# Performance work log

Hardware: AMD Instinct MI355X
Metric: run time of the kernel (lower is better)

Reference implementation:

```python
import jax, jax.numpy as jnp
import numpy as np

N_ITEMS = 30000
D = 128            # embedding_dim
F = D // 2 + 1     # freq_dim = 65
RAW_IMG = 1024
RAW_TXT = 768


def setup_inputs() -> dict:
    key = jax.random.key(0)
    ks = jax.random.split(key, 13)
    return {
        "image_embeds": jax.random.normal(ks[0], (N_ITEMS, D), jnp.float32),
        "text_embeds": jax.random.normal(ks[1], (N_ITEMS, D), jnp.float32),
        "image_table": jax.random.normal(ks[2], (N_ITEMS, RAW_IMG), jnp.float32),
        "text_table": jax.random.normal(ks[3], (N_ITEMS, RAW_TXT), jnp.float32),
        "W_img": jax.random.normal(ks[4], (RAW_IMG, D), jnp.float32) * 0.02,
        "b_img": jax.random.normal(ks[5], (D,), jnp.float32) * 0.02,
        "W_txt": jax.random.normal(ks[6], (RAW_TXT, D), jnp.float32) * 0.02,
        "b_txt": jax.random.normal(ks[7], (D,), jnp.float32) * 0.02,
        "avrf_img": jax.random.normal(ks[8], (F,), jnp.float32),
        "avrf_txt": jax.random.normal(ks[9], (F,), jnp.float32),
        "avg_R": jax.random.normal(ks[10], (F,), jnp.float32),
        "psi": jax.random.normal(ks[11], (F,), jnp.float32) * 0.1,
        "lambda_weights": jnp.array([0.6, 0.4], jnp.float32),
    }


def reference(image_embeds, text_embeds, image_table, text_table,
              W_img, b_img, W_txt, b_txt,
              avrf_img, avrf_txt, avg_R, psi, lambda_weights):
    # project full embedding tables: [N, raw] @ [raw, D] -> [N, D]
    proj_image = image_table @ W_img + b_img
    proj_txt = text_table @ W_txt + b_txt
    # per-row rFFT -> [N, F] complex
    img_fft = jnp.fft.rfft(proj_image, axis=1, norm="ortho")
    txt_fft = jnp.fft.rfft(proj_txt, axis=1, norm="ortho")
    # phase alignment rotation
    phi = avg_R * 0.5 + psi                      # [F]
    rot = jnp.exp(-1j * phi.astype(jnp.complex64))
    APC_img = img_fft * rot[None, :]
    APC_txt = txt_fft * jnp.conj(rot)[None, :]
    # AVRF (variance-ratio) masking -- torch forward uses the raw logit params
    img_vr = APC_img * avrf_img[None, :]
    txt_vr = APC_txt * avrf_txt[None, :]
    # IMCF: magnitude-squared coherence masking
    cross = APC_img * jnp.conj(APC_txt)
    msc = jnp.abs(cross) ** 2 / (jnp.abs(APC_img) ** 2 * jnp.abs(APC_txt) ** 2 + 1e-8)
    img_imcf = APC_img * msc
    txt_imcf = APC_txt * msc
    # softmax-weighted late fusion of the two filtered spectra
    lam = jax.nn.softmax(lambda_weights)
    img_late = lam[0] * img_vr + lam[1] * img_imcf
    txt_late = lam[0] * txt_vr + lam[1] * txt_imcf
    image_conv = jnp.fft.irfft(img_late, n=image_embeds.shape[1], axis=1, norm="ortho")
    text_conv = jnp.fft.irfft(txt_late, n=text_embeds.shape[1], axis=1, norm="ortho")
    return image_conv, text_conv
```

## Files before the change

### kernel.cpp

```cpp
#include <hip/hip_runtime.h>
#include <math.h>

typedef __bf16 bf16x8 __attribute__((ext_vector_type(8)));
typedef float f32x4 __attribute__((ext_vector_type(4)));
typedef unsigned short u16;
typedef unsigned int u32;

#define S128 0.08838834764831845f
#define TWOPI_128 0.04908738521234052f
#define MROWS 30016

__device__ __align__(16) u16 g_wft[56 * 12288];
__device__ __align__(16) u16 g_gt[6 * 8192];
__device__ __align__(16) float g_fp[96 * 8];
__device__ __align__(16) u32 g_S[(size_t)2 * 6 * 4 * MROWS * 8];

__device__ __forceinline__ void split2(float v, u16& h, u16& l) {
  unsigned u = __float_as_uint(v);
  h = (u16)(u >> 16);
  float hf = __uint_as_float(u & 0xFFFF0000u);
  float lo = v - hf;
  unsigned ul = __float_as_uint(lo);
  l = (u16)((ul + 0x7FFFu + ((ul >> 16) & 1u)) >> 16);
}

__device__ __forceinline__ void gll16(const void* gsrc, void* ldst) {
  __builtin_amdgcn_global_load_lds(
      (const __attribute__((address_space(1))) unsigned int*)gsrc,
      (__attribute__((address_space(3))) unsigned int*)ldst, 16, 0, 0);
}

__global__ void k_setup_wft(const float* __restrict__ Wimg,
                            const float* __restrict__ Wtxt, int Kimg, int Ktxt) {
  int gid = blockIdx.x * 256 + threadIdx.x;
  int imgn = Kimg * 96;
  if (gid >= imgn + Ktxt * 96) return;
  const float* Wrow;
  u16* base;
  int kloc, fq;
  if (gid < imgn) {
    kloc = gid / 96; fq = gid % 96;
    Wrow = Wimg + (size_t)kloc * 128;
    base = g_wft + (size_t)(kloc >> 5) * 12288;
  } else {
    int l = gid - imgn;
    kloc = l / 96; fq = l % 96;
    Wrow = Wtxt + (size_t)kloc * 128;
    base = g_wft + (size_t)(32 + (kloc >> 5)) * 12288;
  }
  float re = 0.f, im = 0.f;
  if (fq <= 64) {
    float sts, stc;
    sincosf(TWOPI_128 * (float)fq, &sts, &stc);
    for (int d0 = 0; d0 < 128; d0 += 16) {
      int m = (fq * d0) & 127;
      float sa, ca;
      sincosf(TWOPI_128 * (float)m, &sa, &ca);
      float cr = ca, ci = -sa;
      float wv[16];
      *(float4*)&wv[0]  = *(const float4*)&Wrow[d0];
      *(float4*)&wv[4]  = *(const float4*)&Wrow[d0 + 4];
      *(float4*)&wv[8]  = *(const float4*)&Wrow[d0 + 8];
      *(float4*)&wv[12] = *(const float4*)&Wrow[d0 + 12];
#pragma unroll
      for (int jj = 0; jj < 16; ++jj) {
        re = fmaf(wv[jj], cr, re);
        im = fmaf(wv[jj], ci, im);
        float nc = cr * stc + ci * sts;
        ci = ci * stc - cr * sts;
        cr = nc;
      }
    }
    re *= S128; im *= S128;
  }
  int gran = (kloc & 31) >> 3, j = kloc & 7;
  int cre = (fq >> 4) * 32 + (fq & 15);
  u16 h, l;
  split2(re, h, l);
  base[gran * 1536 + cre * 8 + j] = h;
  base[6144 + gran * 1536 + cre * 8 + j] = l;
  split2(im, h, l);
  base[gran * 1536 + (cre + 16) * 8 + j] = h;
  base[6144 + gran * 1536 + (cre + 16) * 8 + j] = l;
}

__global__ void k_setup_gt(void) {
  int gid = blockIdx.x * 256 + threadIdx.x;
  if (gid >= 192 * 128) return;
  int pk = gid >> 7, n = gid & 127;
  int ks = pk >> 5, w = pk & 31, gran = (w >> 3) & 3, j = w & 7;
  int part = w >> 4, fl = ks * 16 + (w & 15);
  float val = 0.f;
  if (fl <= 64) {
    float ck = (fl == 0 || fl == 64) ? 1.f : 2.f;
    int m = (fl * n) & 127;
    float sa, ca;
    sincosf(TWOPI_128 * (float)m, &sa, &ca);
    val = (part == 0 ? ca : -sa) * ck * S128;
  }
  u16 h, l;
  split2(val, h, l);
  g_gt[ks * 8192 + gran * 1024 + n * 8 + j] = h;
  g_gt[ks * 8192 + 4096 + gran * 1024 + n * 8 + j] = l;
}

__global__ void k_setup_fp(const float* __restrict__ b_img, const float* __restrict__ b_txt,
                           const float* __restrict__ avrf_img, const float* __restrict__ avrf_txt,
                           const float* __restrict__ avg_R, const float* __restrict__ psi) {
  int gid = blockIdx.x * 256 + threadIdx.x;
  if (gid >= 96 * 4) return;
  int k = gid >> 2, q = gid & 3;
  float* fp = g_fp + k * 8;
  if (k > 64) {
    if (q == 0) { fp[0] = 1.f; fp[1] = 0.f; fp[2] = 0.f; fp[3] = 0.f; }
    fp[4 + q] = 0.f;
    return;
  }
  if (q == 0) {
    float phi = avg_R[k] * 0.5f + psi[k];
    float s, c;
    sincosf(phi, &s, &c);
    fp[0] = c; fp[1] = s; fp[2] = avrf_img[k]; fp[3] = avrf_txt[k];
  }
  const float* b = (q < 2) ? b_img : b_txt;
  int part = q & 1;
  float acc = 0.f;
  for (int d = 0; d < 128; ++d) {
    int m = (k * d) & 127;
    float sa, ca;
    sincosf(TWOPI_128 * (float)m, &sa, &ca);
    acc = fmaf(b[d], part ? -sa : ca, acc);
  }
  fp[4 + q] = acc * S128;
}

__global__ __launch_bounds__(256) void k1_gemm(
    const float* __restrict__ Aimg, const float* __restrict__ Atxt,
    int M, int Kimg, int Ktxt, int bpm) {
  __shared__ __align__(16) u16 Asm[2 * 4096];
  __shared__ __align__(16) u16 Bsm[2 * 6144];

  const int bid = blockIdx.x;
  const int mod = bid >= bpm;
  const int bblk = mod ? bid - bpm : bid;
  const float* A = mod ? Atxt : Aimg;
  const int K = mod ? Ktxt : Kimg;
  const u16* wft = g_wft + (mod ? (size_t)32 * 12288 : 0);
  const int row0 = bblk * 64;

  const int tid = threadIdx.x;
  const int lane = tid & 63, wv = tid >> 6;
  const int la = lane & 15, hh = lane >> 4;
  const int wr = wv >> 1, wc = wv & 1;

  const int rseg = tid >> 2, kseg = (tid & 3) * 8;
  int grow = row0 + rseg;
  if (grow > M - 1) grow = M - 1;
  const float* Abase = A + (size_t)grow * K + kseg;

  f32x4 acc[2][6];
#pragma unroll
  for (int rt = 0; rt < 2; ++rt)
#pragma unroll
    for (int ct = 0; ct < 6; ++ct) acc[rt][ct] = (f32x4){0.f, 0.f, 0.f, 0.f};

  const int nst = K / 32;
  float4 av0 = *(const float4*)(Abase);
  float4 av1 = *(const float4*)(Abase + 4);

  for (int s = 0; s < nst; ++s) {
    __syncthreads();
    {
      u16 h8[8], l8[8];
      const float va[8] = {av0.x, av0.y, av0.z, av0.w, av1.x, av1.y, av1.z, av1.w};
#pragma unroll
      for (int j = 0; j < 8; ++j) split2(va[j], h8[j], l8[j]);
      const int ab = (kseg >> 3) * 512 + rseg * 8;
      *(bf16x8*)&Asm[ab] = *(bf16x8*)h8;
      *(bf16x8*)&Asm[4096 + ab] = *(bf16x8*)l8;
    }
    {
      const u16* src = wft + (size_t)s * 12288;
#pragma unroll
      for (int i = 0; i < 6; ++i)
        gll16(src + i * 2048 + tid * 8, (char*)Bsm + i * 4096 + tid * 16);
    }
    __syncthreads();
    if (s + 1 < nst) {
      av0 = *(const float4*)(Abase + (s + 1) * 32);
      av1 = *(const float4*)(Abase + (s + 1) * 32 + 4);
    }
    bf16x8 fah[2], fal[2];
#pragma unroll
    for (int rt = 0; rt < 2; ++rt) {
      const int ar = wr * 32 + rt * 16 + la;
      fah[rt] = *(const bf16x8*)&Asm[hh * 512 + ar * 8];
      fal[rt] = *(const bf16x8*)&Asm[4096 + hh * 512 + ar * 8];
    }
#pragma unroll
    for (int ct = 0; ct < 6; ++ct) {
      const int col = wc * 96 + ct * 16 + la;
      const u16* bb = &Bsm[hh * 1536 + col * 8];
      const bf16x8 fbh = *(const bf16x8*)bb;
      const bf16x8 fbl = *(const bf16x8*)(bb + 6144);
#pragma unroll
      for (int rt = 0; rt < 2; ++rt) {
        acc[rt][ct] = __builtin_amdgcn_mfma_f32_16x16x32_bf16(fah[rt], fbh, acc[rt][ct], 0, 0, 0);
        acc[rt][ct] = __builtin_amdgcn_mfma_f32_16x16x32_bf16(fah[rt], fbl, acc[rt][ct], 0, 0, 0);
        acc[rt][ct] = __builtin_amdgcn_mfma_f32_16x16x32_bf16(fal[rt], fbh, acc[rt][ct], 0, 0, 0);
      }
    }
  }

#pragma unroll
  for (int ct = 0; ct < 6; ++ct) {
    const int cg = wc * 6 + ct;
    const int fq = (cg >> 1) * 16 + la;
    const float bv = g_fp[fq * 8 + 4 + mod * 2 + (cg & 1)];
    const int ks = cg >> 1;
    const int khh = (cg & 1) * 2 + (la >> 3);
    const int j8 = la & 7;
    const size_t sbase = ((size_t)((mod * 6 + ks) * 4 + khh)) * MROWS;
#pragma unroll
    for (int rt = 0; rt < 2; ++rt) {
      const int rb = row0 + wr * 32 + rt * 16 + hh * 4;
#pragma unroll
      for (int j = 0; j < 4; ++j) {
        u16 h, l;
        split2(acc[rt][ct][j] + bv, h, l);
        g_S[(sbase + rb + j) * 8 + j8] = ((u32)h << 16) | l;
      }
    }
  }
}

__global__ __launch_bounds__(256) void k2_idft(
    const float* __restrict__ lamw, float* __restrict__ out, int M) {
  __shared__ __align__(16) u16 Gs[8192];
  __shared__ __align__(16) float fps[96 * 8];

  const int tid = threadIdx.x;
  const int lane = tid & 63, wv = tid >> 6;
  const int la = lane & 15, hh = lane >> 4;
  const int part = hh >> 1;
  const int row = blockIdx.x * 64 + wv * 16 + la;

  if (tid < 192) gll16((const char*)g_fp + tid * 16, (char*)fps + tid * 16);

  const float l0 = lamw[0], l1 = lamw[1];
  const float mx = fmaxf(l0, l1);
  const float e0 = expf(l0 - mx), e1 = expf(l1 - mx);
  const float lam0 = e0 / (e0 + e1), lam1 = e1 / (e0 + e1);

  f32x4 ai[8], at[8];
#pragma unroll
  for (int ct = 0; ct < 8; ++ct) {
    ai[ct] = (f32x4){0.f, 0.f, 0.f, 0.f};
    at[ct] = (f32x4){0.f, 0.f, 0.f, 0.f};
  }

  for (int ks = 0; ks < 6; ++ks) {
    const u32* si = &g_S[((size_t)((0 + ks) * 4 + hh) * MROWS + row) * 8];
    const u32* st = &g_S[((size_t)((24 + ks * 4) + hh) * MROWS + row) * 8];
    uint4 vi0 = *(const uint4*)si, vi1 = *(const uint4*)(si + 4);
    uint4 vt0 = *(const uint4*)st, vt1 = *(const uint4*)(st + 4);

    __syncthreads();
#pragma unroll
    for (int i = 0; i < 4; ++i)
      gll16((const char*)(g_gt + ks * 8192) + i * 4096 + tid * 16,
            (char*)Gs + i * 4096 + tid * 16);
    __syncthreads();

    u32 vs_i[8], vs_t[8];
    *(uint4*)&vs_i[0] = vi0; *(uint4*)&vs_i[4] = vi1;
    *(uint4*)&vs_t[0] = vt0; *(uint4*)&vs_t[4] = vt1;

    const int fq0 = ks * 16 + (hh & 1) * 8;
    u16 yih[8], yil[8], yth[8], ytl[8];
#pragma unroll
    for (int j = 0; j < 8; ++j) {
      const f32x4 fpv = *(const f32x4*)&fps[(fq0 + j) * 8];
      const float o_i = __uint_as_float(vs_i[j] & 0xFFFF0000u) + __uint_as_float(vs_i[j] << 16);
      const float o_t = __uint_as_float(vs_t[j] & 0xFFFF0000u) + __uint_as_float(vs_t[j] << 16);
      const float p_i = __shfl_xor(o_i, 32);
      const float p_t = __shfl_xor(o_t, 32);
      const float Sre_i = part ? p_i : o_i;
      const float Sim_i = part ? o_i : p_i;
      const float Sre_t = part ? p_t : o_t;
      const float Sim_t = part ? o_t : p_t;
      const float rc = fpv[0], rs = fpv[1];
      const float Air = Sre_i * rc + Sim_i * rs, Aii = Sim_i * rc - Sre_i * rs;
      const float Atr = Sre_t * rc - Sim_t * rs, Ati = Sim_t * rc + Sre_t * rs;
      const float cre = Air * Atr + Aii * Ati, cim = Aii * Atr - Air * Ati;
      const float pa = Air * Air + Aii * Aii, pb = Atr * Atr + Ati * Ati;
      const float msc = (cre * cre + cim * cim) / (pa * pb + 1e-8f);
      const float mi = lam0 * fpv[2] + lam1 * msc;
      const float mt = lam0 * fpv[3] + lam1 * msc;
      const float yi = (part ? Aii : Air) * mi;
      const float yt = (part ? Ati : Atr) * mt;
      split2(yi, yih[j], yil[j]);
      split2(yt, yth[j], ytl[j]);
    }
    const bf16x8 fih = *(bf16x8*)yih, fil = *(bf16x8*)yil;
    const bf16x8 fth = *(bf16x8*)yth, ftl = *(bf16x8*)ytl;
#pragma unroll
    for (int ct = 0; ct < 8; ++ct) {
      const u16* gb = &Gs[hh * 1024 + (ct * 16 + la) * 8];
      const bf16x8 gh = *(const bf16x8*)gb;
      const bf16x8 gl = *(const bf16x8*)(gb + 4096);
      ai[ct] = __builtin_amdgcn_mfma_f32_16x16x32_bf16(fih, gh, ai[ct], 0, 0, 0);
      ai[ct] = __builtin_amdgcn_mfma_f32_16x16x32_bf16(fih, gl, ai[ct], 0, 0, 0);
      ai[ct] = __builtin_amdgcn_mfma_f32_16x16x32_bf16(fil, gh, ai[ct], 0, 0, 0);
      at[ct] = __builtin_amdgcn_mfma_f32_16x16x32_bf16(fth, gh, at[ct], 0, 0, 0);
      at[ct] = __builtin_amdgcn_mfma_f32_16x16x32_bf16(fth, gl, at[ct], 0, 0, 0);
      at[ct] = __builtin_amdgcn_mfma_f32_16x16x32_bf16(ftl, gh, at[ct], 0, 0, 0);
    }
  }

  float* oimg = out;
  float* otxt = out + (size_t)M * 128;
#pragma unroll
  for (int q = 0; q < 4; ++q) {
    const int orow = blockIdx.x * 64 + wv * 16 + hh * 4 + q;
    if (orow < M) {
#pragma unroll
      for (int ct = 0; ct < 8; ++ct) {
        oimg[(size_t)orow * 128 + ct * 16 + la] = ai[ct][q];
        otxt[(size_t)orow * 128 + ct * 16 + la] = at[ct][q];
      }
    }
  }
}

extern "C" void kernel_launch(void* const* d_in, const int* in_sizes, int n_in,
                              void* d_out, int out_size, void* d_ws, size_t ws_size,
                              hipStream_t stream) {
  const float* image_table = (const float*)d_in[2];
  const float* text_table  = (const float*)d_in[3];
  const float* W_img = (const float*)d_in[4];
  const float* b_img = (const float*)d_in[5];
  const float* W_txt = (const float*)d_in[6];
  const float* b_txt = (const float*)d_in[7];
  const float* avrf_img = (const float*)d_in[8];
  const float* avrf_txt = (const float*)d_in[9];
  const float* avg_R = (const float*)d_in[10];
  const float* psi = (const float*)d_in[11];
  const float* lamw = (const float*)d_in[12];

  const int M = in_sizes[0] / 128;
  const int K_img = in_sizes[4] / 128;
  const int K_txt = in_sizes[6] / 128;

  const int wft_threads = (K_img + K_txt) * 96;
  k_setup_wft<<<(wft_threads + 255) / 256, 256, 0, stream>>>(W_img, W_txt, K_img, K_txt);
  k_setup_gt<<<(192 * 128 + 255) / 256, 256, 0, stream>>>();
  k_setup_fp<<<2, 256, 0, stream>>>(b_img, b_txt, avrf_img, avrf_txt, avg_R, psi);

  const int bpm = (M + 63) / 64;
  k1_gemm<<<2 * bpm, 256, 0, stream>>>(image_table, text_table, M, K_img, K_txt, bpm);
  k2_idft<<<bpm, 256, 0, stream>>>(lamw, (float*)d_out, M);
}
```

Baseline: 149.5 us.

## Double-buffer B tiles in GEMM and XOR-swizzle LDS layouts against bank conflicts

The GEMM stage now keeps two B (weight-Fourier) tile buffers in LDS and prefetches the next k-step's tile with async global-to-LDS loads while the current step computes, instead of loading and waiting inside each step. The A tile buffer is halved to a single hi/lo pair. The LDS layouts for A, B and the inverse-DFT matrix G get an XOR swizzle on the granule index, applied consistently in the setup kernels that pre-lay-out the weights, to cut LDS bank conflicts on the bf16x8 fragment reads. This costs more LDS per block, which may lower occupancy.

New measurement: 159.7 us. 6.8% more time.

```diff
diff --git a/kernel.cpp b/kernel.cpp
--- a/kernel.cpp
+++ b/kernel.cpp
@@ -77,11 +77,11 @@
   int cre = (fq >> 4) * 32 + (fq & 15);
   u16 h, l;
   split2(re, h, l);
-  base[gran * 1536 + cre * 8 + j] = h;
-  base[6144 + gran * 1536 + cre * 8 + j] = l;
+  base[(gran * 1536 + cre * 8 + j) ^ (gran << 4)] = h;
+  base[6144 + ((gran * 1536 + cre * 8 + j) ^ (gran << 4))] = l;
   split2(im, h, l);
-  base[gran * 1536 + (cre + 16) * 8 + j] = h;
-  base[6144 + gran * 1536 + (cre + 16) * 8 + j] = l;
+  base[(gran * 1536 + (cre + 16) * 8 + j) ^ (gran << 4)] = h;
+  base[6144 + ((gran * 1536 + (cre + 16) * 8 + j) ^ (gran << 4))] = l;
 }
 
 __global__ void k_setup_gt(void) {
@@ -100,8 +100,8 @@
   }
   u16 h, l;
   split2(val, h, l);
-  g_gt[ks * 8192 + gran * 1024 + n * 8 + j] = h;
-  g_gt[ks * 8192 + 4096 + gran * 1024 + n * 8 + j] = l;
+  g_gt[ks * 8192 + ((gran * 1024 + n * 8 + j) ^ (gran << 4))] = h;
+  g_gt[ks * 8192 + 4096 + ((gran * 1024 + n * 8 + j) ^ (gran << 4))] = l;
 }
 
 __global__ void k_setup_fp(const float* __restrict__ b_img, const float* __restrict__ b_txt,
@@ -137,8 +137,8 @@
 __global__ __launch_bounds__(256) void k1_gemm(
     const float* __restrict__ Aimg, const float* __restrict__ Atxt,
     int M, int Kimg, int Ktxt, int bpm) {
-  __shared__ __align__(16) u16 Asm[2 * 4096];
-  __shared__ __align__(16) u16 Bsm[2 * 6144];
+  __shared__ __align__(16) u16 Asm[4096];
+  __shared__ __align__(16) u16 Bsm[2 * 12288];
 
   const int bid = blockIdx.x;
   const int mod = bid >= bpm;
@@ -153,10 +153,11 @@
   const int la = lane & 15, hh = lane >> 4;
   const int wr = wv >> 1, wc = wv & 1;
 
-  const int rseg = tid >> 2, kseg = (tid & 3) * 8;
+  const int rseg = tid >> 2, g4 = tid & 3;
+  const int awoff = (g4 * 512 + rseg * 8) ^ (g4 << 4);
   int grow = row0 + rseg;
   if (grow > M - 1) grow = M - 1;
-  const float* Abase = A + (size_t)grow * K + kseg;
+  const float* Abase = A + (size_t)grow * K + g4 * 8;
 
   f32x4 acc[2][6];
 #pragma unroll
@@ -165,42 +166,50 @@
     for (int ct = 0; ct < 6; ++ct) acc[rt][ct] = (f32x4){0.f, 0.f, 0.f, 0.f};
 
   const int nst = K / 32;
+
+  auto stageB = [&](int s, int buf) {
+    const u16* src = wft + (size_t)s * 12288;
+    char* dst = (char*)Bsm + buf * 24576;
+#pragma unroll
+    for (int i = 0; i < 6; ++i)
+      gll16(src + i * 2048 + tid * 8, dst + i * 4096 + tid * 16);
+  };
+
+  stageB(0, 0);
   float4 av0 = *(const float4*)(Abase);
   float4 av1 = *(const float4*)(Abase + 4);
 
   for (int s = 0; s < nst; ++s) {
+    const int cur = s & 1;
     __syncthreads();
     {
       u16 h8[8], l8[8];
       const float va[8] = {av0.x, av0.y, av0.z, av0.w, av1.x, av1.y, av1.z, av1.w};
 #pragma unroll
       for (int j = 0; j < 8; ++j) split2(va[j], h8[j], l8[j]);
-      const int ab = (kseg >> 3) * 512 + rseg * 8;
-      *(bf16x8*)&Asm[ab] = *(bf16x8*)h8;
-      *(bf16x8*)&Asm[4096 + ab] = *(bf16x8*)l8;
-    }
-    {
-      const u16* src = wft + (size_t)s * 12288;
-#pragma unroll
-      for (int i = 0; i < 6; ++i)
-        gll16(src + i * 2048 + tid * 8, (char*)Bsm + i * 4096 + tid * 16);
+      *(bf16x8*)&Asm[awoff] = *(bf16x8*)h8;
+      *(bf16x8*)&Asm[2048 + awoff] = *(bf16x8*)l8;
     }
     __syncthreads();
+
     if (s + 1 < nst) {
+      stageB(s + 1, cur ^ 1);
       av0 = *(const float4*)(Abase + (s + 1) * 32);
       av1 = *(const float4*)(Abase + (s + 1) * 32 + 4);
     }
+
     bf16x8 fah[2], fal[2];
 #pragma unroll
     for (int rt = 0; rt < 2; ++rt) {
       const int ar = wr * 32 + rt * 16 + la;
-      fah[rt] = *(const bf16x8*)&Asm[hh * 512 + ar * 8];
-      fal[rt] = *(const bf16x8*)&Asm[4096 + hh * 512 + ar * 8];
+      const int off = (hh * 512 + ar * 8) ^ (hh << 4);
+      fah[rt] = *(const bf16x8*)&Asm[off];
+      fal[rt] = *(const bf16x8*)&Asm[2048 + off];
     }
 #pragma unroll
     for (int ct = 0; ct < 6; ++ct) {
       const int col = wc * 96 + ct * 16 + la;
-      const u16* bb = &Bsm[hh * 1536 + col * 8];
+      const u16* bb = &Bsm[cur * 12288 + ((hh * 1536 + col * 8) ^ (hh << 4))];
       const bf16x8 fbh = *(const bf16x8*)bb;
       const bf16x8 fbl = *(const bf16x8*)(bb + 6144);
 #pragma unroll
@@ -306,9 +315,9 @@
     const bf16x8 fth = *(bf16x8*)yth, ftl = *(bf16x8*)ytl;
 #pragma unroll
     for (int ct = 0; ct < 8; ++ct) {
-      const u16* gb = &Gs[hh * 1024 + (ct * 16 + la) * 8];
-      const bf16x8 gh = *(const bf16x8*)gb;
-      const bf16x8 gl = *(const bf16x8*)(gb + 4096);
+      const int goff = (hh * 1024 + (ct * 16 + la) * 8) ^ (hh << 4);
+      const bf16x8 gh = *(const bf16x8*)&Gs[goff];
+      const bf16x8 gl = *(const bf16x8*)&Gs[4096 + goff];
       ai[ct] = __builtin_amdgcn_mfma_f32_16x16x32_bf16(fih, gh, ai[ct], 0, 0, 0);
       ai[ct] = __builtin_amdgcn_mfma_f32_16x16x32_bf16(fih, gl, ai[ct], 0, 0, 0);
       ai[ct] = __builtin_amdgcn_mfma_f32_16x16x32_bf16(fil, gh, ai[ct], 0, 0, 0);
```
